# Performance work log

Hardware: AMD Instinct MI355X
Metric: run time of the kernel (lower is better)

## Reference

```python
import jax, jax.numpy as jnp
import numpy as np

B, T, HID = 2, 1024, 2048
H, DK, DV = 16, 128, 128
KC = 4          # short-conv kernel size
CHUNK = 64
EPS = 1e-5


def _dwconv_silu(x, w):
    # causal depthwise conv1d + SiLU: x [B,T,C], w [C,K]
    K = w.shape[1]
    xp = jnp.pad(x, ((0, 0), (K - 1, 0), (0, 0)))
    y = sum(xp[:, i:i + x.shape[1], :] * w[:, i] for i in range(K))
    return jax.nn.silu(y)


def _l2norm(x):
    return x * jax.lax.rsqrt(jnp.sum(x * x, -1, keepdims=True) + 1e-6)


def setup_inputs() -> dict:
    key = jax.random.key(0)
    ks = jax.random.split(key, 22)
    std = 0.02
    w = lambda k, s: jax.random.normal(k, s, jnp.float32) * std
    return dict(
        hidden_states=jax.random.normal(ks[0], (B, T, HID), jnp.float32),
        Wq=w(ks[1], (HID, H * DK)),
        Wk=w(ks[2], (HID, H * DK)),
        Wv=w(ks[3], (HID, H * DV)),
        conv_wq=w(ks[4], (H * DK, KC)),
        conv_wk=w(ks[5], (H * DK, KC)),
        conv_wv=w(ks[6], (H * DV, KC)),
        Wgb1=w(ks[7], (HID, DV)), Wgb2=w(ks[8], (DV, H * DK)),
        Wgd1=w(ks[9], (HID, DV)), Wgd2=w(ks[10], (DV, H * DK)),
        Wbb=w(ks[11], (HID, H)), Wbd=w(ks[12], (HID, H)),
        Wlam=w(ks[13], (HID, H)),
        A_log=jnp.log(jax.random.uniform(ks[14], (H,), jnp.float32, 1.0, 16.0)),
        dt_bias=jnp.zeros((H * DK,), jnp.float32),
        Wg1=w(ks[15], (HID, DV)), Wg2=w(ks[16], (DV, H * DV)),
        bg2=jnp.zeros((H * DV,), jnp.float32),
        onorm_w=jnp.ones((DV,), jnp.float32),
        Wo=w(ks[17], (H * DV, HID)),
    )


def _fkda_core(q, k, v, gf, gs, bf, bs):
    # dual-state (fast/slow) gated delta rule.
    # q,k: [B,T,H,DK]; v: [B,T,H,DV]; gf/gs: log-decay [B,T,H,DK]; bf/bs: [B,T,H]
    scale = DK ** -0.5
    tm = lambda x: jnp.moveaxis(x, 1, 0)                 # time-major
    qT, kT, vT = tm(q) * scale, tm(k), tm(v)
    g2 = jnp.stack([tm(gf), tm(gs)], 1)                  # [T,2,B,H,DK]
    b2 = jnp.stack([tm(bf), tm(bs)], 1)                  # [T,2,B,H]
    NC = T // CHUNK
    chunkify = lambda x: x.reshape((NC, CHUNK) + x.shape[1:])
    inputs = tuple(map(chunkify, (qT, kT, vT, g2, b2)))

    def step(S, inp):
        qt, kt, vt, gt, bt = inp                         # S: [2,B,H,DK,DV]
        S = S * jnp.exp(gt)[..., None]                   # per-channel decay on key dim
        mem = jnp.einsum('bhk,sbhkv->sbhv', kt, S)       # current memory readout
        u = bt[..., None] * (vt[None] - mem)             # delta-rule residual write
        S = S + jnp.einsum('bhk,sbhv->sbhkv', kt, u)
        o = jnp.einsum('bhk,sbhkv->sbhv', qt, S)
        return S, o

    @jax.checkpoint
    def chunk_step(S, inp):
        return jax.lax.scan(step, S, inp)

    S0 = jnp.zeros((2, q.shape[0], H, DK, DV), q.dtype)
    _, o = jax.lax.scan(chunk_step, S0, inputs)          # [NC,CHUNK,2,B,H,DV]
    o = o.reshape((T,) + o.shape[2:])
    return jnp.moveaxis(o[:, 0], 0, 1), jnp.moveaxis(o[:, 1], 0, 1)


def reference(hidden_states, Wq, Wk, Wv, conv_wq, conv_wk, conv_wv,
              Wgb1, Wgb2, Wgd1, Wgd2, Wbb, Wbd, Wlam, A_log, dt_bias,
              Wg1, Wg2, bg2, onorm_w, Wo):
    x = hidden_states
    b, t, _ = x.shape
    q = _dwconv_silu(x @ Wq, conv_wq).reshape(b, t, H, DK)
    k = _dwconv_silu(x @ Wk, conv_wk).reshape(b, t, H, DK)
    v = _dwconv_silu(x @ Wv, conv_wv).reshape(b, t, H, DV)
    g_base = ((x @ Wgb1) @ Wgb2).reshape(b, t, H, DK)    # low-rank decay gates
    g_delta = ((x @ Wgd1) @ Wgd2).reshape(b, t, H, DK)
    bb, bd = x @ Wbb, x @ Wbd
    lam = jax.nn.sigmoid(x @ Wlam)                       # [b,t,H] fast/slow mix
    beta_fast = jax.nn.sigmoid(bb + bd)
    beta_slow = jax.nn.sigmoid(bb - bd)
    dtb = dt_bias.reshape(H, DK)
    gate_of = lambda g: -jnp.exp(A_log)[None, None, :, None] * jax.nn.softplus(g + dtb)
    gf = gate_of(g_base + g_delta)                       # fused_kda_gate, fast
    gs = gate_of(g_base - g_delta)                       # slow (share_decay_gate=False)
    q, k = _l2norm(q), _l2norm(k)                        # use_qk_l2norm_in_kernel
    o_f, o_s = _fkda_core(q, k, v, gf, gs, beta_fast, beta_slow)
    o = lam[..., None] * o_f + (1.0 - lam[..., None]) * o_s
    gate = ((x @ Wg1) @ Wg2 + bg2).reshape(b, t, H, DV)
    o = o * jax.lax.rsqrt(jnp.mean(o * o, -1, keepdims=True) + EPS) * onorm_w
    o = o * jax.nn.sigmoid(gate)                         # FusedRMSNormGated(sigmoid)
    return o.reshape(b, t, H * DV) @ Wo
```

## Files before the change

### kernel.cpp

```cpp
#include <hip/hip_runtime.h>
#include <hip/hip_bf16.h>
#include <math.h>
#include <stdint.h>

#define B_   2
#define T_   1024
#define HID_ 2048
#define H_   16
#define DK_  128
#define DV_  128
#define TS_  16

typedef __bf16 bf16;
typedef __attribute__((ext_vector_type(8))) __bf16 bf16x8;
typedef __attribute__((ext_vector_type(4))) float f32x4;

typedef __attribute__((address_space(3))) uint32_t* lds_ptr_t;
typedef const __attribute__((address_space(1))) uint32_t* glb_ptr_t;

__device__ __forceinline__ float sigmoidf_(float x) {
    return 1.0f / (1.0f + __expf(-x));
}

__device__ __forceinline__ void ldg_to_lds16(const void* g, void* lds) {
    __builtin_amdgcn_global_load_lds((glb_ptr_t)(uintptr_t)g,
                                     (lds_ptr_t)(uintptr_t)lds, 16, 0, 0);
}

template <int CTRL>
__device__ __forceinline__ float dpp_ror_add(float x) {
    int yi = __builtin_amdgcn_update_dpp(
        0, __builtin_bit_cast(int, x), CTRL, 0xF, 0xF, true);
    return x + __builtin_bit_cast(float, yi);
}
__device__ __forceinline__ float row16_allreduce(float x) {
    x = dpp_ror_add<0x128>(x);
    x = dpp_ror_add<0x124>(x);
    x = dpp_ror_add<0x122>(x);
    x = dpp_ror_add<0x121>(x);
    return x;
}

__global__ __launch_bounds__(256) void cast_bf16_kernel(
    const float* __restrict__ in, bf16* __restrict__ out)
{
    int i = blockIdx.x * 256 + threadIdx.x;
    float4 a = ((const float4*)in)[2 * i];
    float4 b = ((const float4*)in)[2 * i + 1];
    bf16x8 o;
    o[0] = (bf16)a.x; o[1] = (bf16)a.y; o[2] = (bf16)a.z; o[3] = (bf16)a.w;
    o[4] = (bf16)b.x; o[5] = (bf16)b.y; o[6] = (bf16)b.z; o[7] = (bf16)b.w;
    ((bf16x8*)out)[i] = o;
}

__global__ __launch_bounds__(256) void tcast_kernel(
    const float* __restrict__ W, bf16* __restrict__ Wt, int K, int N)
{
    __shared__ float tile[32][33];
    const int k0 = blockIdx.y * 32, n0 = blockIdx.x * 32;
    const int r = threadIdx.x >> 5, c = threadIdx.x & 31;
    #pragma unroll
    for (int i = 0; i < 4; ++i)
        tile[r + 8 * i][c] = W[(size_t)(k0 + r + 8 * i) * N + n0 + c];
    __syncthreads();
    #pragma unroll
    for (int i = 0; i < 4; ++i)
        Wt[(size_t)(n0 + r + 8 * i) * K + k0 + c] = (bf16)tile[c][r + 8 * i];
}

__global__ __launch_bounds__(256) void tcast_off_kernel(
    const float* __restrict__ W, bf16* __restrict__ Wt,
    int N, int noff, int koff, float sign)
{
    __shared__ float tile[32][33];
    const int k0 = blockIdx.y * 32, n0 = blockIdx.x * 32;
    const int r = threadIdx.x >> 5, c = threadIdx.x & 31;
    #pragma unroll
    for (int i = 0; i < 4; ++i)
        tile[r + 8 * i][c] = W[(size_t)(k0 + r + 8 * i) * N + n0 + c];
    __syncthreads();
    #pragma unroll
    for (int i = 0; i < 4; ++i)
        Wt[(size_t)(noff + n0 + r + 8 * i) * 256 + koff + k0 + c] =
            (bf16)(sign * tile[c][r + 8 * i]);
}

__global__ __launch_bounds__(256) void mfma_gemm_kernel(
    const bf16* __restrict__ A, const bf16* __restrict__ Bt,
    const float* __restrict__ bias, void* __restrict__ Cout,
    int M, int N, int Kfull, int lda, int ldc, int bf16out)
{
    __shared__ bf16 As[128 * 32];
    __shared__ bf16 Bs[128 * 32];

    const int tid  = threadIdx.x;
    const int w    = tid >> 6;
    const int lane = tid & 63;
    const int n0   = blockIdx.x * 128;
    const int m0   = blockIdx.y * 128;
    const int wm   = (w >> 1) * 64;
    const int wn   = (w & 1) * 64;

    const int lr = lane >> 2;
    const int lc = (lane & 3) * 8;

    f32x4 acc[4][4];
    #pragma unroll
    for (int i = 0; i < 4; ++i)
        #pragma unroll
        for (int j = 0; j < 4; ++j) acc[i][j] = (f32x4)0.0f;

    const bf16* ApL = As + (wm + (lane & 15)) * 32 + (lane >> 4) * 8;
    const bf16* BpL = Bs + (wn + (lane & 15)) * 32 + (lane >> 4) * 8;

    for (int k0 = 0; k0 < Kfull; k0 += 32) {
        #pragma unroll
        for (int i = 0; i < 2; ++i) {
            const int rr = (w * 2 + i) * 16 + lr;
            ldg_to_lds16(A  + (size_t)(m0 + rr) * lda   + k0 + lc, As + (w * 2 + i) * 512);
            ldg_to_lds16(Bt + (size_t)(n0 + rr) * Kfull + k0 + lc, Bs + (w * 2 + i) * 512);
        }
        __syncthreads();

        bf16x8 af[4], bfr[4];
        #pragma unroll
        for (int i = 0; i < 4; ++i) af[i]  = *(const bf16x8*)(ApL + i * 16 * 32);
        #pragma unroll
        for (int j = 0; j < 4; ++j) bfr[j] = *(const bf16x8*)(BpL + j * 16 * 32);
        #pragma unroll
        for (int i = 0; i < 4; ++i)
            #pragma unroll
            for (int j = 0; j < 4; ++j)
                acc[i][j] = __builtin_amdgcn_mfma_f32_16x16x32_bf16(
                    af[i], bfr[j], acc[i][j], 0, 0, 0);
        __syncthreads();
    }

    #pragma unroll
    for (int i = 0; i < 4; ++i) {
        const int row = m0 + wm + i * 16 + (lane >> 4) * 4;
        #pragma unroll
        for (int j = 0; j < 4; ++j) {
            const int col = n0 + wn + j * 16 + (lane & 15);
            const float bv = bias ? bias[col] : 0.0f;
            #pragma unroll
            for (int r = 0; r < 4; ++r) {
                float v = acc[i][j][r] + bv;
                if (bf16out) ((bf16*)Cout)[(size_t)(row + r) * ldc + col] = (bf16)v;
                else ((float*)Cout)[(size_t)(row + r) * ldc + col] = v;
            }
        }
    }
}

__global__ __launch_bounds__(256) void midcast_kernel(
    const float* __restrict__ src, bf16* __restrict__ midb)
{
    int i = blockIdx.x * 256 + threadIdx.x;
    int m = i / 96, c4 = i - m * 96;
    float4 v = *(const float4*)(src + (size_t)m * 6528 + 6144 + c4 * 4);
    bf16 o[4] = {(bf16)v.x, (bf16)v.y, (bf16)v.z, (bf16)v.w};
    *(uint64_t*)(midb + (size_t)m * 384 + c4 * 4) = *(uint64_t*)o;
}

__global__ __launch_bounds__(256) void skinny3_kernel(
    const float* __restrict__ x, const float* __restrict__ Wbb,
    const float* __restrict__ Wbd, const float* __restrict__ Wlam,
    float* __restrict__ bb, float* __restrict__ bd, float* __restrict__ lam)
{
    __shared__ float xs[16][128];
    __shared__ float wsh[128][48];
    const int m0  = blockIdx.x * 16;
    const int tid = threadIdx.x;
    const int r = tid >> 4, cg = tid & 15;
    float acc0 = 0.f, acc1 = 0.f, acc2 = 0.f;

    for (int k0 = 0; k0 < HID_; k0 += 128) {
        __syncthreads();
        #pragma unroll
        for (int i = 0; i < 2; ++i) {
            int f = tid + 256 * i;
            int rr = f >> 5, cc = (f & 31) * 4;
            *(float4*)&xs[rr][cc] = *(const float4*)(x + (size_t)(m0 + rr) * HID_ + k0 + cc);
        }
        #pragma unroll
        for (int i = 0; i < 2; ++i) {
            int f = tid + 256 * i;
            int kk = f >> 2, cc = (f & 3) * 4;
            *(float4*)&wsh[kk][cc]      = *(const float4*)(Wbb  + (size_t)(k0 + kk) * 16 + cc);
            *(float4*)&wsh[kk][16 + cc] = *(const float4*)(Wbd  + (size_t)(k0 + kk) * 16 + cc);
            *(float4*)&wsh[kk][32 + cc] = *(const float4*)(Wlam + (size_t)(k0 + kk) * 16 + cc);
        }
        __syncthreads();
        #pragma unroll 8
        for (int kk = 0; kk < 128; ++kk) {
            float xv = xs[r][kk];
            acc0 += xv * wsh[kk][cg];
            acc1 += xv * wsh[kk][16 + cg];
            acc2 += xv * wsh[kk][32 + cg];
        }
    }
    size_t o = (size_t)(m0 + r) * 16 + cg;
    bb[o] = acc0; bd[o] = acc1; lam[o] = acc2;
}

__global__ __launch_bounds__(256) void conv_silu_kernel(
    const float* __restrict__ xin, int ldx, int coloff,
    const float* __restrict__ w, float* __restrict__ yout, int mode)
{
    const int bt  = blockIdx.x;
    const int t   = bt & (T_ - 1);
    const int tid = threadIdx.x;
    const float* xr = xin + (size_t)bt * ldx + coloff;

    float val[8];
    #pragma unroll
    for (int jj = 0; jj < 8; ++jj) {
        int c = tid + 256 * jj;
        float4 wc = *(const float4*)(w + (size_t)c * 4);
        const float* xc = xr + c;
        float acc = wc.w * xc[0];
        if (t >= 1) acc += wc.z * xc[-ldx];
        if (t >= 2) acc += wc.y * xc[-2 * ldx];
        if (t >= 3) acc += wc.x * xc[-3 * ldx];
        val[jj] = acc * sigmoidf_(acc);
    }

    if (mode > 0) {
        __shared__ float red[4][8];
        const int wv = tid >> 6;
        #pragma unroll
        for (int jj = 0; jj < 8; ++jj) {
            float v2 = val[jj] * val[jj];
            #pragma unroll
            for (int m = 1; m < 64; m <<= 1) v2 += __shfl_xor(v2, m);
            if ((tid & 63) == 0) red[wv][jj] = v2;
        }
        __syncthreads();
        const int wb = (tid >> 7) * 2;
        #pragma unroll
        for (int jj = 0; jj < 8; ++jj) {
            float ss = red[wb][jj] + red[wb + 1][jj];
            float sc = rsqrtf(ss + 1e-6f);
            if (mode == 2) sc *= 0.08838834764831845f;
            val[jj] *= sc;
        }
    }

    const size_t row = (size_t)bt * HID_;
    #pragma unroll
    for (int jj = 0; jj < 8; ++jj)
        yout[row + tid + 256 * jj] = val[jj];
}

__global__ __launch_bounds__(256) void decay_gate_kernel(
    float* gfgs, const float* __restrict__ A_log,
    const float* __restrict__ dt_bias)
{
    size_t i = (size_t)blockIdx.x * 256 + threadIdx.x;
    int c = (int)(i & (HID_ - 1));
    size_t m = i >> 11;
    int h = c >> 7;
    float* pf = gfgs + m * 4096 + c;
    float* ps = pf + 2048;
    float na = -__expf(A_log[h]);
    float db = dt_bias[c];
    float xf = *pf + db;
    float xs = *ps + db;
    float spf = (xf > 20.0f) ? xf : log1pf(__expf(xf));
    float sps = (xs > 20.0f) ? xs : log1pf(__expf(xs));
    *pf = __expf(na * spf);
    *ps = __expf(na * sps);
}

__global__ __launch_bounds__(256) void fkda_kernel(
    const float* __restrict__ qp, const float* __restrict__ kp,
    const float* __restrict__ vp, const float* __restrict__ egf,
    const float* __restrict__ egs, int ldeg,
    const float* __restrict__ bbp, const float* __restrict__ bdp,
    float* __restrict__ ofp, float* __restrict__ osp)
{
    const int bx = blockIdx.x;
    const int bh = bx & 31;
    const int sv = bx >> 5;
    const int b  = bh >> 4;
    const int h  = bh & 15;
    const int s  = sv >> 3;
    const int vc = sv & 7;

    const float* eg = s ? egs : egf;
    float*       op = s ? osp : ofp;
    const float  bsign = s ? -1.0f : 1.0f;

    const int tid  = threadIdx.x;
    const int lane = tid & 63;
    const int w    = tid >> 6;
    const int kseg = lane & 15;
    const int colb = w * 4 + (lane >> 4);

    const size_t base  = (size_t)b * T_ * HID_ + (size_t)h * DK_;
    const size_t baseg = (size_t)b * T_ * ldeg + (size_t)h * DK_;

    __shared__ float EG[TS_ * 128];
    __shared__ float KK[TS_ * 128];
    __shared__ float QQ[TS_ * 128];
    __shared__ float VV[TS_ * 16];
    __shared__ float OT[TS_ * 16];
    __shared__ float BT[TS_];

    float S[8];
    #pragma unroll
    for (int j = 0; j < 8; ++j) S[j] = 0.0f;

    const int l5  = lane & 31;
    const int ttl = lane >> 5;
    const int cg  = (l5 < 16) ? (l5 * 8) : ((l5 - 16) * 8 + 4);
    const int sl  = kseg * 4;

    for (int t0 = 0; t0 < T_; t0 += TS_) {
        #pragma unroll
        for (int i = 0; i < 2; ++i) {
            int n  = w * 2 + i;
            int tt = n * 2 + ttl;
            size_t rq = base  + (size_t)(t0 + tt) * HID_ + cg;
            size_t rg = baseg + (size_t)(t0 + tt) * ldeg + cg;
            ldg_to_lds16(eg + rg, EG + n * 256);
            ldg_to_lds16(kp + rq, KK + n * 256);
            ldg_to_lds16(qp + rq, QQ + n * 256);
        }
        if (tid < 64) {
            int tt = tid >> 2, vo = (tid & 3) * 4;
            size_t g = base + (size_t)(t0 + tt) * HID_ + vc * 16 + vo;
            ((float4*)VV)[tid] = *(const float4*)(vp + g);
        }
        if (tid < TS_) {
            size_t gi = ((size_t)b * T_ + t0 + tid) * H_ + h;
            BT[tid] = sigmoidf_(bbp[gi] + bsign * bdp[gi]);
        }
        __syncthreads();

        #pragma unroll
        for (int tt = 0; tt < TS_; ++tt) {
            float e[8], kf[8], qf[8];
            *(float4*)&e[0]  = *(const float4*)(EG + tt * 128 + sl);
            *(float4*)&e[4]  = *(const float4*)(EG + tt * 128 + 64 + sl);
            *(float4*)&kf[0] = *(const float4*)(KK + tt * 128 + sl);
            *(float4*)&kf[4] = *(const float4*)(KK + tt * 128 + 64 + sl);
            *(float4*)&qf[0] = *(const float4*)(QQ + tt * 128 + sl);
            *(float4*)&qf[4] = *(const float4*)(QQ + tt * 128 + 64 + sl);
            float vcol = VV[tt * 16 + colb];
            float btv  = BT[tt];

            float p0 = 0.0f, p1 = 0.0f;
            #pragma unroll
            for (int j = 0; j < 8; j += 2) {
                S[j]     *= e[j];     p0 += kf[j]     * S[j];
                S[j + 1] *= e[j + 1]; p1 += kf[j + 1] * S[j + 1];
            }
            float p = row16_allreduce(p0 + p1);

            float u = btv * (vcol - p);

            float o0 = 0.0f, o1 = 0.0f;
            #pragma unroll
            for (int j = 0; j < 8; j += 2) {
                S[j]     += kf[j]     * u; o0 += qf[j]     * S[j];
                S[j + 1] += kf[j + 1] * u; o1 += qf[j + 1] * S[j + 1];
            }
            float oo = row16_allreduce(o0 + o1);

            if (kseg == 0) OT[tt * 16 + colb] = oo;
        }
        __syncthreads();

        if (tid < 64) {
            int tt = tid >> 2, vo = (tid & 3) * 4;
            size_t g = base + (size_t)(t0 + tt) * HID_ + vc * 16 + vo;
            *(float4*)(op + g) = ((const float4*)OT)[tid];
        }
    }
}

__global__ __launch_bounds__(256) void mix_norm_gate_kernel(
    const float* of, const float* os, const float* lam_pre,
    const float* gate, const float* onorm_w, bf16* outp)
{
    const int bt  = blockIdx.x;
    const int tid = threadIdx.x;
    const size_t row = (size_t)bt * HID_;

    float val[8];
    #pragma unroll
    for (int jj = 0; jj < 8; ++jj) {
        int c = tid + 256 * jj;
        int h = c >> 7;
        float l = sigmoidf_(lam_pre[(size_t)bt * H_ + h]);
        val[jj] = l * of[row + c] + (1.0f - l) * os[row + c];
    }

    __shared__ float red[4][8];
    const int wv = tid >> 6;
    #pragma unroll
    for (int jj = 0; jj < 8; ++jj) {
        float v2 = val[jj] * val[jj];
        #pragma unroll
        for (int m = 1; m < 64; m <<= 1) v2 += __shfl_xor(v2, m);
        if ((tid & 63) == 0) red[wv][jj] = v2;
    }
    __syncthreads();
    const int wb = (tid >> 7) * 2;
    #pragma unroll
    for (int jj = 0; jj < 8; ++jj) {
        int c = tid + 256 * jj;
        float ss   = red[wb][jj] + red[wb + 1][jj];
        float mean = ss * (1.0f / 128.0f);
        float sc   = rsqrtf(mean + 1e-5f) * onorm_w[c & 127];
        float g    = sigmoidf_(gate[row + c]);
        outp[row + c] = (bf16)(val[jj] * sc * g);
    }
}

extern "C" void kernel_launch(void* const* d_in, const int* in_sizes, int n_in,
                              void* d_out, int out_size, void* d_ws, size_t ws_size,
                              hipStream_t stream) {
    const float* x       = (const float*)d_in[0];
    const float* Wq      = (const float*)d_in[1];
    const float* Wk      = (const float*)d_in[2];
    const float* Wv      = (const float*)d_in[3];
    const float* conv_wq = (const float*)d_in[4];
    const float* conv_wk = (const float*)d_in[5];
    const float* conv_wv = (const float*)d_in[6];
    const float* Wgb1    = (const float*)d_in[7];
    const float* Wgb2    = (const float*)d_in[8];
    const float* Wgd1    = (const float*)d_in[9];
    const float* Wgd2    = (const float*)d_in[10];
    const float* Wbb     = (const float*)d_in[11];
    const float* Wbd     = (const float*)d_in[12];
    const float* Wlam    = (const float*)d_in[13];
    const float* A_log   = (const float*)d_in[14];
    const float* dt_bias = (const float*)d_in[15];
    const float* Wg1     = (const float*)d_in[16];
    const float* Wg2     = (const float*)d_in[17];
    const float* bg2     = (const float*)d_in[18];
    const float* onorm_w = (const float*)d_in[19];
    const float* Wo      = (const float*)d_in[20];
    float* out = (float*)d_out;

    const size_t M = (size_t)B_ * T_;

    float* ws = (float*)d_ws;
    size_t off = 0;
    auto alloc = [&](size_t nfloats) { float* p = ws + off; off += nfloats; return p; };

    float* bufQKV = alloc(M * 6528);
    float* wqkvTf = alloc((size_t)6528 * HID_ / 2);
    float* xbf    = alloc(M * HID_ / 2);
    float* bufQ   = alloc(M * HID_);
    float* bufK   = alloc(M * HID_);
    float* bufV   = alloc(M * HID_);
    float* bufC   = alloc(M * HID_);
    float* bufD   = alloc(M * HID_);
    float* midbf  = alloc(M * 384 / 2);
    float* bb     = alloc(M * H_);
    float* bd     = alloc(M * H_);
    float* lamp   = alloc(M * H_);

    bf16* xb    = (bf16*)xbf;
    bf16* obf   = (bf16*)xbf;
    bf16* wqkvT = (bf16*)wqkvTf;
    bf16* woT   = wqkvT;
    bf16* wcat  = wqkvT + (size_t)HID_ * HID_;
    bf16* wgate = wcat + (size_t)4096 * 256;
    bf16* midb  = (bf16*)midbf;
    float* gfgs = bufQKV;
    float* bufE = bufQKV + M * 4096;

    dim3 blk(256);
    auto gemm = [&](const bf16* A, const bf16* Bt, const float* bias, void* C,
                    int Mm, int Nn, int Kk, int lda, int ldc, int bf16out) {
        dim3 grid(Nn / 128, Mm / 128);
        mfma_gemm_kernel<<<grid, blk, 0, stream>>>(A, Bt, bias, C, Mm, Nn, Kk,
                                                   lda, ldc, bf16out);
    };
    auto tcast = [&](const float* W, bf16* Wt, int Kk, int Nn) {
        tcast_kernel<<<dim3(Nn / 32, Kk / 32), blk, 0, stream>>>(W, Wt, Kk, Nn);
    };

    cast_bf16_kernel<<<dim3((unsigned)(M * HID_ / 8 / 256)), blk, 0, stream>>>(x, xb);

    tcast(Wq,   wqkvT,                          HID_, HID_);
    tcast(Wk,   wqkvT + (size_t)2048 * HID_,    HID_, HID_);
    tcast(Wv,   wqkvT + (size_t)4096 * HID_,    HID_, HID_);
    tcast(Wgb1, wqkvT + (size_t)6144 * HID_,    HID_, 128);
    tcast(Wgd1, wqkvT + (size_t)6272 * HID_,    HID_, 128);
    tcast(Wg1,  wqkvT + (size_t)6400 * HID_,    HID_, 128);
    gemm(xb, wqkvT, nullptr, bufQKV, (int)M, 6528, HID_, HID_, 6528, 0);

    conv_silu_kernel<<<dim3(B_ * T_), blk, 0, stream>>>(bufQKV, 6528, 0,
        conv_wq, bufQ, 2);
    conv_silu_kernel<<<dim3(B_ * T_), blk, 0, stream>>>(bufQKV, 6528, 2048,
        conv_wk, bufK, 1);
    conv_silu_kernel<<<dim3(B_ * T_), blk, 0, stream>>>(bufQKV, 6528, 4096,
        conv_wv, bufV, 0);

    midcast_kernel<<<dim3((unsigned)(M * 96 / 256)), blk, 0, stream>>>(bufQKV, midb);

    skinny3_kernel<<<dim3((unsigned)(M / 16)), blk, 0, stream>>>(
        x, Wbb, Wbd, Wlam, bb, bd, lamp);

    tcast_off_kernel<<<dim3(64, 4), blk, 0, stream>>>(Wgb2, wcat, HID_, 0,    0,   1.0f);
    tcast_off_kernel<<<dim3(64, 4), blk, 0, stream>>>(Wgd2, wcat, HID_, 0,    128, 1.0f);
    tcast_off_kernel<<<dim3(64, 4), blk, 0, stream>>>(Wgb2, wcat, HID_, 2048, 0,   1.0f);
    tcast_off_kernel<<<dim3(64, 4), blk, 0, stream>>>(Wgd2, wcat, HID_, 2048, 128, -1.0f);
    tcast(Wg2, wgate, 128, HID_);
    tcast(Wo,  woT,   HID_, HID_);
    gemm(midb,       wcat,  nullptr, gfgs, (int)M, 4096, 256, 384, 4096, 0);
    gemm(midb + 256, wgate, bg2,     bufE, (int)M, HID_, 128, 384, HID_, 0);

    decay_gate_kernel<<<dim3((unsigned)(M * HID_ / 256)), blk, 0, stream>>>(
        gfgs, A_log, dt_bias);

    fkda_kernel<<<dim3(512), blk, 0, stream>>>(bufQ, bufK, bufV,
        gfgs, gfgs + 2048, 4096, bb, bd, bufC, bufD);

    mix_norm_gate_kernel<<<dim3(B_ * T_), blk, 0, stream>>>(
        bufC, bufD, lamp, bufE, onorm_w, obf);

    gemm(obf, woT, nullptr, out, (int)M, HID_, HID_, HID_, HID_, 0);
}
```

Measured before the change: 751.1 us.

## Store q/k in bf16 and process two value columns per thread in fkda

The conv kernel now writes normalized q and k as bf16, halving their global and LDS footprint. The recurrent fkda kernel gives each thread two value columns (S0/S1), so each k/q/decay load from LDS is reused twice. The grid shrinks from 512 to 256 blocks, each covering 32 value columns. This cuts load traffic and reduction overhead per unit of work, but lowers parallelism on a latency-bound sequential scan and adds bf16 rounding to q and k.

```diff
diff --git a/kernel.cpp b/kernel.cpp
--- a/kernel.cpp
+++ b/kernel.cpp
@@ -206,7 +206,8 @@
 
 __global__ __launch_bounds__(256) void conv_silu_kernel(
     const float* __restrict__ xin, int ldx, int coloff,
-    const float* __restrict__ w, float* __restrict__ yout, int mode)
+    const float* __restrict__ w,
+    bf16* __restrict__ ybf, float* __restrict__ yf32, int mode)
 {
     const int bt  = blockIdx.x;
     const int t   = bt & (T_ - 1);
@@ -248,9 +249,15 @@
     }
 
     const size_t row = (size_t)bt * HID_;
-    #pragma unroll
-    for (int jj = 0; jj < 8; ++jj)
-        yout[row + tid + 256 * jj] = val[jj];
+    if (mode == 0) {
+        #pragma unroll
+        for (int jj = 0; jj < 8; ++jj)
+            yf32[row + tid + 256 * jj] = val[jj];
+    } else {
+        #pragma unroll
+        for (int jj = 0; jj < 8; ++jj)
+            ybf[row + tid + 256 * jj] = (bf16)val[jj];
+    }
 }
 
 __global__ __launch_bounds__(256) void decay_gate_kernel(
@@ -274,7 +281,7 @@
 }
 
 __global__ __launch_bounds__(256) void fkda_kernel(
-    const float* __restrict__ qp, const float* __restrict__ kp,
+    const bf16* __restrict__ qp, const bf16* __restrict__ kp,
     const float* __restrict__ vp, const float* __restrict__ egf,
     const float* __restrict__ egs, int ldeg,
     const float* __restrict__ bbp, const float* __restrict__ bdp,
@@ -285,52 +292,57 @@
     const int sv = bx >> 5;
     const int b  = bh >> 4;
     const int h  = bh & 15;
-    const int s  = sv >> 3;
-    const int vc = sv & 7;
+    const int s  = sv >> 2;
+    const int vc = sv & 3;
 
     const float* eg = s ? egs : egf;
     float*       op = s ? osp : ofp;
     const float  bsign = s ? -1.0f : 1.0f;
 
-    const int tid  = threadIdx.x;
-    const int lane = tid & 63;
-    const int w    = tid >> 6;
-    const int kseg = lane & 15;
-    const int colb = w * 4 + (lane >> 4);
+    const int tid   = threadIdx.x;
+    const int lane  = tid & 63;
+    const int w     = tid >> 6;
+    const int kseg  = lane & 15;
+    const int colg  = lane >> 4;
+    const int cpair = w * 8 + colg * 2;
 
     const size_t base  = (size_t)b * T_ * HID_ + (size_t)h * DK_;
     const size_t baseg = (size_t)b * T_ * ldeg + (size_t)h * DK_;
 
     __shared__ float EG[TS_ * 128];
-    __shared__ float KK[TS_ * 128];
-    __shared__ float QQ[TS_ * 128];
-    __shared__ float VV[TS_ * 16];
-    __shared__ float OT[TS_ * 16];
+    __shared__ bf16  KK[TS_ * 128];
+    __shared__ bf16  QQ[TS_ * 128];
+    __shared__ float VV[TS_ * 32];
+    __shared__ float OT[TS_ * 32];
     __shared__ float BT[TS_];
 
-    float S[8];
-    #pragma unroll
-    for (int j = 0; j < 8; ++j) S[j] = 0.0f;
+    float S0[8], S1[8];
+    #pragma unroll
+    for (int j = 0; j < 8; ++j) { S0[j] = 0.0f; S1[j] = 0.0f; }
 
     const int l5  = lane & 31;
     const int ttl = lane >> 5;
     const int cg  = (l5 < 16) ? (l5 * 8) : ((l5 - 16) * 8 + 4);
     const int sl  = kseg * 4;
 
+    const int krow = w * 4 + (lane >> 4);
+    const int kcol = (lane & 15) * 8;
+
     for (int t0 = 0; t0 < T_; t0 += TS_) {
         #pragma unroll
         for (int i = 0; i < 2; ++i) {
             int n  = w * 2 + i;
             int tt = n * 2 + ttl;
-            size_t rq = base  + (size_t)(t0 + tt) * HID_ + cg;
-            size_t rg = baseg + (size_t)(t0 + tt) * ldeg + cg;
-            ldg_to_lds16(eg + rg, EG + n * 256);
-            ldg_to_lds16(kp + rq, KK + n * 256);
-            ldg_to_lds16(qp + rq, QQ + n * 256);
-        }
-        if (tid < 64) {
-            int tt = tid >> 2, vo = (tid & 3) * 4;
-            size_t g = base + (size_t)(t0 + tt) * HID_ + vc * 16 + vo;
+            ldg_to_lds16(eg + baseg + (size_t)(t0 + tt) * ldeg + cg, EG + n * 256);
+        }
+        {
+            size_t g = base + (size_t)(t0 + krow) * HID_ + kcol;
+            ldg_to_lds16(kp + g, KK + w * 512);
+            ldg_to_lds16(qp + g, QQ + w * 512);
+        }
+        if (tid < 128) {
+            int tt = tid >> 3, vo = (tid & 7) * 4;
+            size_t g = base + (size_t)(t0 + tt) * HID_ + vc * 32 + vo;
             ((float4*)VV)[tid] = *(const float4*)(vp + g);
         }
         if (tid < TS_) {
@@ -341,41 +353,53 @@
 
         #pragma unroll
         for (int tt = 0; tt < TS_; ++tt) {
-            float e[8], kf[8], qf[8];
-            *(float4*)&e[0]  = *(const float4*)(EG + tt * 128 + sl);
-            *(float4*)&e[4]  = *(const float4*)(EG + tt * 128 + 64 + sl);
-            *(float4*)&kf[0] = *(const float4*)(KK + tt * 128 + sl);
-            *(float4*)&kf[4] = *(const float4*)(KK + tt * 128 + 64 + sl);
-            *(float4*)&qf[0] = *(const float4*)(QQ + tt * 128 + sl);
-            *(float4*)&qf[4] = *(const float4*)(QQ + tt * 128 + 64 + sl);
-            float vcol = VV[tt * 16 + colb];
-            float btv  = BT[tt];
-
-            float p0 = 0.0f, p1 = 0.0f;
+            float e[8];
+            *(float4*)&e[0] = *(const float4*)(EG + tt * 128 + sl);
+            *(float4*)&e[4] = *(const float4*)(EG + tt * 128 + 64 + sl);
+            bf16x8 k8 = *(const bf16x8*)(KK + tt * 128 + kseg * 8);
+            bf16x8 q8 = *(const bf16x8*)(QQ + tt * 128 + kseg * 8);
+            float2 v2 = *(const float2*)(VV + tt * 32 + cpair);
+            float btv = BT[tt];
+
+            float kf[8], qf[8];
+            #pragma unroll
+            for (int j = 0; j < 8; ++j) { kf[j] = (float)k8[j]; qf[j] = (float)q8[j]; }
+
+            float p0a = 0.f, p0b = 0.f, p1a = 0.f, p1b = 0.f;
             #pragma unroll
             for (int j = 0; j < 8; j += 2) {
-                S[j]     *= e[j];     p0 += kf[j]     * S[j];
-                S[j + 1] *= e[j + 1]; p1 += kf[j + 1] * S[j + 1];
+                S0[j]     *= e[j];     p0a += kf[j]     * S0[j];
+                S0[j + 1] *= e[j + 1]; p0b += kf[j + 1] * S0[j + 1];
+                S1[j]     *= e[j];     p1a += kf[j]     * S1[j];
+                S1[j + 1] *= e[j + 1]; p1b += kf[j + 1] * S1[j + 1];
             }
-            float p = row16_allreduce(p0 + p1);
-
-            float u = btv * (vcol - p);
-
-            float o0 = 0.0f, o1 = 0.0f;
+            float p0 = row16_allreduce(p0a + p0b);
+            float p1 = row16_allreduce(p1a + p1b);
+
+            float u0 = btv * (v2.x - p0);
+            float u1 = btv * (v2.y - p1);
+
+            float o0a = 0.f, o0b = 0.f, o1a = 0.f, o1b = 0.f;
             #pragma unroll
             for (int j = 0; j < 8; j += 2) {
-                S[j]     += kf[j]     * u; o0 += qf[j]     * S[j];
-                S[j + 1] += kf[j + 1] * u; o1 += qf[j + 1] * S[j + 1];
+                S0[j]     += kf[j]     * u0; o0a += qf[j]     * S0[j];
+                S0[j + 1] += kf[j + 1] * u0; o0b += qf[j + 1] * S0[j + 1];
+                S1[j]     += kf[j]     * u1; o1a += qf[j]     * S1[j];
+                S1[j + 1] += kf[j + 1] * u1; o1b += qf[j + 1] * S1[j + 1];
             }
-            float oo = row16_allreduce(o0 + o1);
-
-            if (kseg == 0) OT[tt * 16 + colb] = oo;
-        }
-        __syncthreads();
-
-        if (tid < 64) {
-            int tt = tid >> 2, vo = (tid & 3) * 4;
-            size_t g = base + (size_t)(t0 + tt) * HID_ + vc * 16 + vo;
+            float o0 = row16_allreduce(o0a + o0b);
+            float o1 = row16_allreduce(o1a + o1b);
+
+            if (kseg == 0) {
+                OT[tt * 32 + cpair]     = o0;
+                OT[tt * 32 + cpair + 1] = o1;
+            }
+        }
+        __syncthreads();
+
+        if (tid < 128) {
+            int tt = tid >> 3, vo = (tid & 7) * 4;
+            size_t g = base + (size_t)(t0 + tt) * HID_ + vc * 32 + vo;
             *(float4*)(op + g) = ((const float4*)OT)[tid];
         }
     }
@@ -455,8 +479,8 @@
     float* bufQKV = alloc(M * 6528);
     float* wqkvTf = alloc((size_t)6528 * HID_ / 2);
     float* xbf    = alloc(M * HID_ / 2);
-    float* bufQ   = alloc(M * HID_);
-    float* bufK   = alloc(M * HID_);
+    float* bufQf  = alloc(M * HID_ / 2);
+    float* bufKf  = alloc(M * HID_ / 2);
     float* bufV   = alloc(M * HID_);
     float* bufC   = alloc(M * HID_);
     float* bufD   = alloc(M * HID_);
@@ -467,6 +491,8 @@
 
     bf16* xb    = (bf16*)xbf;
     bf16* obf   = (bf16*)xbf;
+    bf16* bufQ  = (bf16*)bufQf;
+    bf16* bufK  = (bf16*)bufKf;
     bf16* wqkvT = (bf16*)wqkvTf;
     bf16* woT   = wqkvT;
     bf16* wcat  = wqkvT + (size_t)HID_ * HID_;
@@ -497,11 +523,11 @@
     gemm(xb, wqkvT, nullptr, bufQKV, (int)M, 6528, HID_, HID_, 6528, 0);
 
     conv_silu_kernel<<<dim3(B_ * T_), blk, 0, stream>>>(bufQKV, 6528, 0,
-        conv_wq, bufQ, 2);
+        conv_wq, bufQ, nullptr, 2);
     conv_silu_kernel<<<dim3(B_ * T_), blk, 0, stream>>>(bufQKV, 6528, 2048,
-        conv_wk, bufK, 1);
+        conv_wk, bufK, nullptr, 1);
     conv_silu_kernel<<<dim3(B_ * T_), blk, 0, stream>>>(bufQKV, 6528, 4096,
-        conv_wv, bufV, 0);
+        conv_wv, nullptr, bufV, 0);
 
     midcast_kernel<<<dim3((unsigned)(M * 96 / 256)), blk, 0, stream>>>(bufQKV, midb);
 
@@ -520,7 +546,7 @@
     decay_gate_kernel<<<dim3((unsigned)(M * HID_ / 256)), blk, 0, stream>>>(
         gfgs, A_log, dt_bias);
 
-    fkda_kernel<<<dim3(512), blk, 0, stream>>>(bufQ, bufK, bufV,
+    fkda_kernel<<<dim3(256), blk, 0, stream>>>(bufQ, bufK, bufV,
         gfgs, gfgs + 2048, 4096, bb, bd, bufC, bufD);
 
     mix_norm_gate_kernel<<<dim3(B_ * T_), blk, 0, stream>>>(
```

New measurement: 784.6 us. +4.5%, slower.
